# Performance work log

Measured on AMD Instinct MI355X. Metric: run time of the kernel, lower is better.

Reference implementation:

```python
import jax, jax.numpy as jnp
import numpy as np

N, F_IN, H1, H2, HEADS, E = 8192, 512, 128, 64, 3, 262144
NEG_SLOPE = 0.2  # PyG GATConv default negative_slope


def _add_self_loops(src, dst, n):
    loop = jnp.arange(n, dtype=src.dtype)
    return jnp.concatenate([src, loop]), jnp.concatenate([dst, loop])


def _gcn_conv(x, src, dst, W, b, n):
    # PyG GCNConv: h = x @ W, add self-loops, symmetric D^-1/2 A D^-1/2 aggregation, + bias
    h = x @ W
    s, d = _add_self_loops(src, dst, n)
    deg = jax.ops.segment_sum(jnp.ones(s.shape, h.dtype), d, num_segments=n)
    dinv = jnp.where(deg > 0, jax.lax.rsqrt(deg), 0.0)
    norm = dinv[s] * dinv[d]  # [E']
    return jax.ops.segment_sum(h[s] * norm[:, None], d, num_segments=n) + b


def _gat_conv(x, src, dst, W, a_src, a_dst, b, n, heads, concat):
    # PyG GATConv: per-head linear, LeakyReLU attention logits, segment softmax over
    # incoming edges per destination node, weighted scatter-aggregate.
    out_dim = W.shape[1] // heads
    h = (x @ W).reshape(n, heads, out_dim)  # [N, H, D]
    s, d = _add_self_loops(src, dst, n)
    a_s = jnp.einsum('nhd,hd->nh', h, a_src)
    a_d = jnp.einsum('nhd,hd->nh', h, a_dst)
    e = jax.nn.leaky_relu(a_s[s] + a_d[d], NEG_SLOPE)  # [E', H]
    m = jax.ops.segment_max(e, d, num_segments=n)      # stable softmax per dst segment
    ex = jnp.exp(e - m[d])
    den = jax.ops.segment_sum(ex, d, num_segments=n)
    msg = h[s] * (ex / den[d])[..., None]              # [E', H, D]
    out = jax.ops.segment_sum(msg, d, num_segments=n)  # [N, H, D]
    if concat:
        return out.reshape(n, heads * out_dim) + b
    return out.mean(axis=1) + b


def _forward(x, edge_index, gcn_W1, gcn_b1, gcn_Wmu, gcn_bmu, gcn_Wlv, gcn_blv,
             gat_W1, gat_as1, gat_ad1, gat_b1,
             gat_Wmu, gat_asmu, gat_admu, gat_bmu,
             gat_Wlv, gat_aslv, gat_adlv, gat_blv,
             eps_gcn, eps_gat):
    src, dst = edge_index[0], edge_index[1]
    n = x.shape[0]
    mu_g = lv_g = z_g = None
    for i in range(gcn_W1.shape[0]):  # gcn branches
        h = jax.nn.relu(_gcn_conv(x, src, dst, gcn_W1[i], gcn_b1[i], n))
        mu = _gcn_conv(h, src, dst, gcn_Wmu[i], gcn_bmu[i], n)
        lv = _gcn_conv(h, src, dst, gcn_Wlv[i], gcn_blv[i], n)
        z = mu + eps_gcn[i] * jnp.exp(lv)  # faithful: logvar passed as logstd
        mu_g = mu if mu_g is None else jnp.maximum(mu_g, mu)
        lv_g = lv if lv_g is None else jnp.maximum(lv_g, lv)
        z_g = z if z_g is None else jnp.maximum(z_g, z)
    mu_a = lv_a = z_a = None
    for i in range(gat_W1.shape[0]):  # gat branches
        h = jax.nn.relu(_gat_conv(x, src, dst, gat_W1[i], gat_as1[i], gat_ad1[i], gat_b1[i], n, HEADS, True))
        mu = _gat_conv(h, src, dst, gat_Wmu[i], gat_asmu[i], gat_admu[i], gat_bmu[i], n, HEADS, False)
        lv = _gat_conv(h, src, dst, gat_Wlv[i], gat_aslv[i], gat_adlv[i], gat_blv[i], n, HEADS, False)
        z = mu + eps_gat[i] * jnp.exp(lv)
        mu_a = mu if mu_a is None else jnp.maximum(mu_a, mu)
        lv_a = lv if lv_a is None else jnp.maximum(lv_a, lv)
        z_a = z if z_a is None else jnp.maximum(z_a, z)
    mu_max = jnp.maximum(mu_g, mu_a)
    lv_max = jnp.maximum(lv_g, lv_a)
    z_max = jnp.maximum(z_g, z_a)
    adj = jax.nn.sigmoid(z_max @ z_max.T)  # InnerProductDecoder.forward_all(sigmoid=True)
    return adj, mu_max, lv_max


def setup_inputs():
    key = jax.random.key(0)
    ki = iter(jax.random.split(key, 32))
    p = lambda shape: jax.random.normal(next(ki), shape, dtype=jnp.float32) * 0.05
    x = jax.random.normal(next(ki), (N, F_IN), dtype=jnp.float32)
    edge_index = jax.random.randint(next(ki), (2, E), 0, N)
    return dict(
        x=x, edge_index=edge_index,
        gcn_W1=p((2, F_IN, H1)), gcn_b1=p((2, H1)),
        gcn_Wmu=p((2, H1, H2)), gcn_bmu=p((2, H2)),
        gcn_Wlv=p((2, H1, H2)), gcn_blv=p((2, H2)),
        gat_W1=p((2, F_IN, HEADS * H1)), gat_as1=p((2, HEADS, H1)),
        gat_ad1=p((2, HEADS, H1)), gat_b1=p((2, HEADS * H1)),
        gat_Wmu=p((2, HEADS * H1, HEADS * H2)), gat_asmu=p((2, HEADS, H2)),
        gat_admu=p((2, HEADS, H2)), gat_bmu=p((2, H2)),
        gat_Wlv=p((2, HEADS * H1, HEADS * H2)), gat_aslv=p((2, HEADS, H2)),
        gat_adlv=p((2, HEADS, H2)), gat_blv=p((2, H2)),
        eps_gcn=jax.random.normal(next(ki), (2, N, H2), dtype=jnp.float32),
        eps_gat=jax.random.normal(next(ki), (2, N, H2), dtype=jnp.float32),
    )


def reference(x, edge_index, gcn_W1, gcn_b1, gcn_Wmu, gcn_bmu, gcn_Wlv, gcn_blv,
              gat_W1, gat_as1, gat_ad1, gat_b1,
              gat_Wmu, gat_asmu, gat_admu, gat_bmu,
              gat_Wlv, gat_aslv, gat_adlv, gat_blv,
              eps_gcn, eps_gat):
    return _forward(x, edge_index, gcn_W1, gcn_b1, gcn_Wmu, gcn_bmu, gcn_Wlv, gcn_blv,
                    gat_W1, gat_as1, gat_ad1, gat_b1,
                    gat_Wmu, gat_asmu, gat_admu, gat_bmu,
                    gat_Wlv, gat_aslv, gat_adlv, gat_blv,
                    eps_gcn, eps_gat)
```

## Files before the change

kernel.cpp:

```cpp
#include <hip/hip_runtime.h>
#include <hip/hip_bf16.h>
#include <math.h>
#include <stddef.h>

#define NN 8192
#define NEG_SLOPE 0.2f

typedef _Float16 h8 __attribute__((ext_vector_type(8)));
typedef __attribute__((ext_vector_type(4))) float f32x4;

__device__ __forceinline__ float lrelu(float x) { return x > 0.f ? x : NEG_SLOPE * x; }
__device__ __forceinline__ float sigf(float x) { return 1.f / (1.f + __expf(-x)); }

__device__ __forceinline__ unsigned short f16b(float x) {
    _Float16 h = (_Float16)x;
    unsigned short u;
    __builtin_memcpy(&u, &h, 2);
    return u;
}
__device__ __forceinline__ float f16f(unsigned short u) {
    _Float16 h;
    __builtin_memcpy(&h, &u, 2);
    return (float)h;
}
__device__ __forceinline__ void splith(float x, unsigned short& hu, unsigned short& lu) {
    _Float16 h = (_Float16)x;
    float hf = (float)h;
    _Float16 l = (_Float16)(x - hf);
    __builtin_memcpy(&hu, &h, 2);
    __builtin_memcpy(&lu, &l, 2);
}
__device__ __forceinline__ float2 unpkh(unsigned int v) {
    float2 r;
    r.x = f16f((unsigned short)(v & 0xffffu));
    r.y = f16f((unsigned short)(v >> 16));
    return r;
}
__device__ __forceinline__ unsigned int packh(float a, float b) {
    return (unsigned int)f16b(a) | ((unsigned int)f16b(b) << 16);
}

__device__ __forceinline__ void gll16(const unsigned short* g, unsigned short* l) {
    __builtin_amdgcn_global_load_lds(
        (const __attribute__((address_space(1))) unsigned int*)g,
        (__attribute__((address_space(3))) unsigned int*)l, 16, 0, 0);
}

__global__ void k_zero(int* __restrict__ p, int n) {
    int i = blockIdx.x * blockDim.x + threadIdx.x;
    if (i < n) p[i] = 0;
}
__global__ void k_count(const int* __restrict__ dst, int* __restrict__ cnt, int E) {
    int i = blockIdx.x * blockDim.x + threadIdx.x;
    if (i < E) atomicAdd(&cnt[dst[i]], 1);
}
__global__ void k_dinv(const int* __restrict__ cnt, float* __restrict__ dinv) {
    int i = blockIdx.x * blockDim.x + threadIdx.x;
    if (i < NN) dinv[i] = rsqrtf((float)(cnt[i] + 1));
}
__global__ void k_scan(const int* __restrict__ cnt, int* __restrict__ row_ptr) {
    __shared__ int part[1024];
    int t = threadIdx.x;
    int base = t * 8;
    int loc[8];
    int s = 0;
    #pragma unroll
    for (int j = 0; j < 8; ++j) { loc[j] = s; s += cnt[base + j]; }
    part[t] = s;
    __syncthreads();
    for (int off = 1; off < 1024; off <<= 1) {
        int v = (t >= off) ? part[t - off] : 0;
        __syncthreads();
        part[t] += v;
        __syncthreads();
    }
    int pre = (t == 0) ? 0 : part[t - 1];
    #pragma unroll
    for (int j = 0; j < 8; ++j) row_ptr[base + j] = pre + loc[j];
    if (t == 1023) row_ptr[NN] = part[1023];
}
__global__ void k_fill(const int* __restrict__ src, const int* __restrict__ dst,
                       const int* __restrict__ row_ptr, int* __restrict__ cursor,
                       int* __restrict__ csr_src, int E) {
    int i = blockIdx.x * blockDim.x + threadIdx.x;
    if (i < E) {
        int d = dst[i];
        csr_src[row_ptr[d] + atomicAdd(&cursor[d], 1)] = src[i];
    }
}

__global__ void k_cvt_x(const float* __restrict__ x, unsigned short* __restrict__ xh) {
    int i = blockIdx.x * 256 + threadIdx.x;
    int m = i >> 7, k4 = (i & 127) * 4;
    float4 v = *(const float4*)(x + (size_t)m * 512 + k4);
    ushort4 o;
    o.x = f16b(v.x); o.y = f16b(v.y); o.z = f16b(v.z); o.w = f16b(v.w);
    *(ushort4*)&xh[(size_t)m * 512 + k4] = o;
}

__global__ void k_wT(const float* __restrict__ W, unsigned short* __restrict__ Wt,
                     int K, int N, size_t wt_z_stride, int noff, int noff_z) {
    int b = blockIdx.z;
    W += (size_t)b * K * N;
    Wt += (size_t)b * wt_z_stride;
    int rowbase = noff + b * noff_z;
    int k0 = blockIdx.x * 32, n0 = blockIdx.y * 32;
    __shared__ float tl[32][33];
    int tid = threadIdx.x;
    int r = tid >> 5, cc = tid & 31;
    #pragma unroll
    for (int c = 0; c < 4; ++c)
        tl[r + c * 8][cc] = W[(size_t)(k0 + r + c * 8) * N + n0 + cc];
    __syncthreads();
    #pragma unroll
    for (int c = 0; c < 4; ++c) {
        int n = r + c * 8, k = cc;
        Wt[(size_t)(rowbase + n0 + n) * K + k0 + k] = f16b(tl[k][n]);
    }
}

template <int ROWS>
__device__ __forceinline__ void stage(const unsigned short* __restrict__ gbase, int lda,
                                      unsigned short* lds, int wid, int lane) {
    #pragma unroll
    for (int c = 0; c < ROWS / 32; ++c) {
        int chunk = c * 4 + wid;
        int row = chunk * 8 + (lane >> 3);
        int g = (lane & 7) ^ (row & 7);
        gll16(gbase + (size_t)row * lda + g * 8, lds + chunk * 512);
    }
}
__device__ __forceinline__ h8 fragrh(const unsigned short* lds, int row, int kg) {
    return *(const h8*)(lds + row * 64 + ((kg ^ (row & 7)) * 8));
}

template <int TERMS, int EPI>
__global__ __launch_bounds__(256) void k_gemm2(
    const unsigned short* __restrict__ A2, size_t azs, int lda,
    const unsigned short* __restrict__ B2, size_t bzs, int ldb,
    void* __restrict__ Cv, size_t czs, int ldc, int K) {
    __shared__ __align__(16) unsigned short sAh[128 * 64];
    __shared__ __align__(16) unsigned short sBh[64 * 64];
    __shared__ __align__(16) unsigned short sAl[(TERMS == 3) ? 128 * 64 : 8];
    __shared__ __align__(16) unsigned short sBl[(TERMS == 3) ? 64 * 64 : 8];
    const int tid = threadIdx.x;
    const int wid = tid >> 6, lane = tid & 63;
    const int wr = wid >> 1, wc = wid & 1;
    const int lr = lane & 15, lg = lane >> 4;
    const int m0 = blockIdx.x * 128, n0 = blockIdx.y * 64;
    const int z = blockIdx.z;
    A2 += (size_t)z * azs;
    B2 += (size_t)z * bzs;

    const f32x4 zero4 = {0.f, 0.f, 0.f, 0.f};
    f32x4 acc[4][2];
    #pragma unroll
    for (int m = 0; m < 4; ++m)
        #pragma unroll
        for (int n = 0; n < 2; ++n) acc[m][n] = zero4;

    for (int k0 = 0; k0 < K; k0 += 64) {
        stage<128>(A2 + (size_t)m0 * lda + k0, lda, sAh, wid, lane);
        stage<64> (B2 + (size_t)n0 * ldb + k0, ldb, sBh, wid, lane);
        if (TERMS == 3) {
            stage<128>(A2 + (size_t)m0 * lda + K + k0, lda, sAl, wid, lane);
            stage<64> (B2 + (size_t)n0 * ldb + K + k0, ldb, sBl, wid, lane);
        }
        __syncthreads();
        #pragma unroll
        for (int ks = 0; ks < 2; ++ks) {
            const int kg = ks * 4 + lg;
            h8 ah[4], al[4], bh[2], bl[2];
            #pragma unroll
            for (int m = 0; m < 4; ++m) {
                int row = wr * 64 + m * 16 + lr;
                ah[m] = fragrh(sAh, row, kg);
                if (TERMS == 3) al[m] = fragrh(sAl, row, kg);
            }
            #pragma unroll
            for (int n = 0; n < 2; ++n) {
                int row = wc * 32 + n * 16 + lr;
                bh[n] = fragrh(sBh, row, kg);
                if (TERMS == 3) bl[n] = fragrh(sBl, row, kg);
            }
            #pragma unroll
            for (int m = 0; m < 4; ++m)
                #pragma unroll
                for (int n = 0; n < 2; ++n) {
                    acc[m][n] = __builtin_amdgcn_mfma_f32_16x16x32_f16(ah[m], bh[n], acc[m][n], 0, 0, 0);
                    if (TERMS == 3) {
                        acc[m][n] = __builtin_amdgcn_mfma_f32_16x16x32_f16(al[m], bh[n], acc[m][n], 0, 0, 0);
                        acc[m][n] = __builtin_amdgcn_mfma_f32_16x16x32_f16(ah[m], bl[n], acc[m][n], 0, 0, 0);
                    }
                }
        }
        __syncthreads();
    }
    #pragma unroll
    for (int m = 0; m < 4; ++m)
        #pragma unroll
        for (int n = 0; n < 2; ++n)
            #pragma unroll
            for (int j = 0; j < 4; ++j) {
                int row = m0 + wr * 64 + m * 16 + lg * 4 + j;
                int col = n0 + wc * 32 + n * 16 + lr;
                float o = acc[m][n][j];
                if (EPI == 1) {
                    ((float*)Cv + (size_t)z * czs)[(size_t)row * ldc + col] = sigf(o);
                } else if (EPI == 2) {
                    ((unsigned short*)Cv + (size_t)z * czs)[(size_t)row * ldc + col] = f16b(o);
                } else {
                    ((float*)Cv + (size_t)z * czs)[(size_t)row * ldc + col] = o;
                }
            }
}

__global__ void k_gcn_a1(const uint2* __restrict__ xw2, const float* __restrict__ dinv,
                         const int* __restrict__ rp, const int* __restrict__ cs,
                         const float* __restrict__ b1, uint2* __restrict__ hb2) {
    int d = blockIdx.x;
    int t = threadIdx.x;
    float dd = dinv[d];
    uint2 sv = xw2[(size_t)d * 64 + t];
    float2 s0 = unpkh(sv.x), s1 = unpkh(sv.y);
    float a0 = dd * s0.x, a1 = dd * s0.y, a2 = dd * s1.x, a3 = dd * s1.y;
    int e0 = rp[d], e1 = rp[d + 1];
    int j = e0;
    for (; j + 4 <= e1; j += 4) {
        int i0 = cs[j], i1 = cs[j + 1], i2 = cs[j + 2], i3 = cs[j + 3];
        float w0 = dinv[i0], w1 = dinv[i1], w2 = dinv[i2], w3 = dinv[i3];
        uint2 v0 = xw2[(size_t)i0 * 64 + t];
        uint2 v1 = xw2[(size_t)i1 * 64 + t];
        uint2 v2 = xw2[(size_t)i2 * 64 + t];
        uint2 v3 = xw2[(size_t)i3 * 64 + t];
        float2 p;
        p = unpkh(v0.x); a0 += w0 * p.x; a1 += w0 * p.y;
        p = unpkh(v0.y); a2 += w0 * p.x; a3 += w0 * p.y;
        p = unpkh(v1.x); a0 += w1 * p.x; a1 += w1 * p.y;
        p = unpkh(v1.y); a2 += w1 * p.x; a3 += w1 * p.y;
        p = unpkh(v2.x); a0 += w2 * p.x; a1 += w2 * p.y;
        p = unpkh(v2.y); a2 += w2 * p.x; a3 += w2 * p.y;
        p = unpkh(v3.x); a0 += w3 * p.x; a1 += w3 * p.y;
        p = unpkh(v3.y); a2 += w3 * p.x; a3 += w3 * p.y;
    }
    for (; j < e1; ++j) {
        int s = cs[j];
        float w = dinv[s];
        uint2 v = xw2[(size_t)s * 64 + t];
        float2 p;
        p = unpkh(v.x); a0 += w * p.x; a1 += w * p.y;
        p = unpkh(v.y); a2 += w * p.x; a3 += w * p.y;
    }
    int c = 4 * t;
    float o0 = fmaxf(dd * a0 + b1[c], 0.f);
    float o1 = fmaxf(dd * a1 + b1[c + 1], 0.f);
    float o2 = fmaxf(dd * a2 + b1[c + 2], 0.f);
    float o3 = fmaxf(dd * a3 + b1[c + 3], 0.f);
    uint2 o;
    o.x = packh(o0, o1);
    o.y = packh(o2, o3);
    hb2[(size_t)d * 64 + t] = o;
}

__global__ void k_gcn_a2(const uint2* __restrict__ hb2, const float* __restrict__ dinv,
                         const int* __restrict__ rp, const int* __restrict__ cs,
                         uint2* __restrict__ hA2) {
    int d = blockIdx.x;
    int t = threadIdx.x;
    float dd = dinv[d];
    uint2 sv = hb2[(size_t)d * 64 + t];
    float2 s0 = unpkh(sv.x), s1 = unpkh(sv.y);
    float a0 = dd * s0.x, a1 = dd * s0.y, a2 = dd * s1.x, a3 = dd * s1.y;
    int e0 = rp[d], e1 = rp[d + 1];
    int j = e0;
    for (; j + 4 <= e1; j += 4) {
        int i0 = cs[j], i1 = cs[j + 1], i2 = cs[j + 2], i3 = cs[j + 3];
        float w0 = dinv[i0], w1 = dinv[i1], w2 = dinv[i2], w3 = dinv[i3];
        uint2 v0 = hb2[(size_t)i0 * 64 + t];
        uint2 v1 = hb2[(size_t)i1 * 64 + t];
        uint2 v2 = hb2[(size_t)i2 * 64 + t];
        uint2 v3 = hb2[(size_t)i3 * 64 + t];
        float2 p;
        p = unpkh(v0.x); a0 += w0 * p.x; a1 += w0 * p.y;
        p = unpkh(v0.y); a2 += w0 * p.x; a3 += w0 * p.y;
        p = unpkh(v1.x); a0 += w1 * p.x; a1 += w1 * p.y;
        p = unpkh(v1.y); a2 += w1 * p.x; a3 += w1 * p.y;
        p = unpkh(v2.x); a0 += w2 * p.x; a1 += w2 * p.y;
        p = unpkh(v2.y); a2 += w2 * p.x; a3 += w2 * p.y;
        p = unpkh(v3.x); a0 += w3 * p.x; a1 += w3 * p.y;
        p = unpkh(v3.y); a2 += w3 * p.x; a3 += w3 * p.y;
    }
    for (; j < e1; ++j) {
        int s = cs[j];
        float w = dinv[s];
        uint2 v = hb2[(size_t)s * 64 + t];
        float2 p;
        p = unpkh(v.x); a0 += w * p.x; a1 += w * p.y;
        p = unpkh(v.y); a2 += w * p.x; a3 += w * p.y;
    }
    uint2 o;
    o.x = packh(dd * a0, dd * a1);
    o.y = packh(dd * a2, dd * a3);
    hA2[(size_t)d * 64 + t] = o;
}

__global__ void k_gat_log1(const unsigned int* __restrict__ xwu, const float* __restrict__ a_s,
                           const float* __restrict__ a_d, float* __restrict__ as_n,
                           float* __restrict__ ad_n) {
    int br = blockIdx.z;
    int n = blockIdx.x;
    int hd = threadIdx.x >> 6, lane = threadIdx.x & 63;
    const unsigned int* hp = xwu + (size_t)n * 384 + br * 192 + hd * 64;
    const float* av = a_s + br * 384 + hd * 128;
    const float* dv = a_d + br * 384 + hd * 128;
    float2 f = unpkh(hp[lane]);
    float ss = f.x * av[2 * lane] + f.y * av[2 * lane + 1];
    float sd = f.x * dv[2 * lane] + f.y * dv[2 * lane + 1];
    #pragma unroll
    for (int off = 32; off; off >>= 1) {
        ss += __shfl_down(ss, off);
        sd += __shfl_down(sd, off);
    }
    if (lane == 0) {
        as_n[(size_t)br * NN * 3 + n * 3 + hd] = ss;
        ad_n[(size_t)br * NN * 3 + n * 3 + hd] = sd;
    }
}

__global__ void k_gat_log2(const unsigned short* __restrict__ h2gb, const float* __restrict__ asmu,
                           const float* __restrict__ aslv, const float* __restrict__ admu,
                           const float* __restrict__ adlv, float* __restrict__ as_n,
                           float* __restrict__ ad_n) {
    int zz = blockIdx.z;
    int br = zz >> 1, mt = zz & 1;
    int n = blockIdx.x;
    int hd = threadIdx.x >> 6, lane = threadIdx.x & 63;
    const unsigned short* hp = h2gb + (size_t)br * NN * 384 + (size_t)n * 384 + mt * 192 + hd * 64;
    const float* av = (mt ? aslv : asmu) + br * 192 + hd * 64;
    const float* dv = (mt ? adlv : admu) + br * 192 + hd * 64;
    float hv = f16f(hp[lane]);
    float ss = hv * av[lane];
    float sd = hv * dv[lane];
    #pragma unroll
    for (int off = 32; off; off >>= 1) {
        ss += __shfl_down(ss, off);
        sd += __shfl_down(sd, off);
    }
    if (lane == 0) {
        as_n[(size_t)zz * NN * 3 + n * 3 + hd] = ss;
        ad_n[(size_t)zz * NN * 3 + n * 3 + hd] = sd;
    }
}

__global__ void k_gat_attn(const float* __restrict__ as_n, const float* __restrict__ ad_n,
                           const int* __restrict__ rp, const int* __restrict__ cs,
                           float* __restrict__ w_csr, float* __restrict__ w_self, int E3) {
    int zz = blockIdx.z;
    as_n += (size_t)zz * NN * 3;
    ad_n += (size_t)zz * NN * 3;
    w_csr += (size_t)zz * E3;
    w_self += (size_t)zz * NN * 3;
    int d = blockIdx.x;
    int hd = threadIdx.x >> 6, lane = threadIdx.x & 63;
    int e0 = rp[d], e1 = rp[d + 1];
    float add = ad_n[d * 3 + hd];
    float eself = lrelu(as_n[d * 3 + hd] + add);
    float mx = eself;
    for (int j = e0 + lane; j < e1; j += 64) {
        float e = lrelu(as_n[cs[j] * 3 + hd] + add);
        w_csr[(size_t)j * 3 + hd] = e;
        mx = fmaxf(mx, e);
    }
    #pragma unroll
    for (int off = 32; off; off >>= 1) mx = fmaxf(mx, __shfl_xor(mx, off));
    float sm = (lane == 0) ? __expf(eself - mx) : 0.f;
    for (int j = e0 + lane; j < e1; j += 64)
        sm += __expf(w_csr[(size_t)j * 3 + hd] - mx);
    #pragma unroll
    for (int off = 32; off; off >>= 1) sm += __shfl_xor(sm, off);
    float inv = 1.f / sm;
    if (lane == 0) w_self[d * 3 + hd] = __expf(eself - mx) * inv;
    for (int j = e0 + lane; j < e1; j += 64)
        w_csr[(size_t)j * 3 + hd] = __expf(w_csr[(size_t)j * 3 + hd] - mx) * inv;
}

__global__ void k_gat_agg1(const uint2* __restrict__ xw2, const float* __restrict__ w_csr,
                           const float* __restrict__ w_self, const int* __restrict__ rp,
                           const int* __restrict__ cs, const float* __restrict__ b1,
                           uint2* __restrict__ h1s2, int E3) {
    int d = blockIdx.x;
    int t = threadIdx.x;
    int br = t >= 96 ? 1 : 0;
    int c = 4 * t - br * 384;
    int hd = c >> 7;
    const float* wc = w_csr + (size_t)br * E3;
    float ws = w_self[(size_t)br * NN * 3 + d * 3 + hd];
    uint2 sv = xw2[(size_t)d * 192 + t];
    float2 s0 = unpkh(sv.x), s1 = unpkh(sv.y);
    float a0 = ws * s0.x, a1 = ws * s0.y, a2 = ws * s1.x, a3 = ws * s1.y;
    int e0 = rp[d], e1 = rp[d + 1];
    int j = e0;
    for (; j + 4 <= e1; j += 4) {
        int i0 = cs[j], i1 = cs[j + 1], i2 = cs[j + 2], i3 = cs[j + 3];
        float w0 = wc[(size_t)(j + 0) * 3 + hd];
        float w1 = wc[(size_t)(j + 1) * 3 + hd];
        float w2 = wc[(size_t)(j + 2) * 3 + hd];
        float w3 = wc[(size_t)(j + 3) * 3 + hd];
        uint2 v0 = xw2[(size_t)i0 * 192 + t];
        uint2 v1 = xw2[(size_t)i1 * 192 + t];
        uint2 v2 = xw2[(size_t)i2 * 192 + t];
        uint2 v3 = xw2[(size_t)i3 * 192 + t];
        float2 p;
        p = unpkh(v0.x); a0 += w0 * p.x; a1 += w0 * p.y;
        p = unpkh(v0.y); a2 += w0 * p.x; a3 += w0 * p.y;
        p = unpkh(v1.x); a0 += w1 * p.x; a1 += w1 * p.y;
        p = unpkh(v1.y); a2 += w1 * p.x; a3 += w1 * p.y;
        p = unpkh(v2.x); a0 += w2 * p.x; a1 += w2 * p.y;
        p = unpkh(v2.y); a2 += w2 * p.x; a3 += w2 * p.y;
        p = unpkh(v3.x); a0 += w3 * p.x; a1 += w3 * p.y;
        p = unpkh(v3.y); a2 += w3 * p.x; a3 += w3 * p.y;
    }
    for (; j < e1; ++j) {
        int s = cs[j];
        float w = wc[(size_t)j * 3 + hd];
        uint2 v = xw2[(size_t)s * 192 + t];
        float2 p;
        p = unpkh(v.x); a0 += w * p.x; a1 += w * p.y;
        p = unpkh(v.y); a2 += w * p.x; a3 += w * p.y;
    }
    int cg = 4 * t;
    float o0 = fmaxf(a0 + b1[cg], 0.f);
    float o1 = fmaxf(a1 + b1[cg + 1], 0.f);
    float o2 = fmaxf(a2 + b1[cg + 2], 0.f);
    float o3 = fmaxf(a3 + b1[cg + 3], 0.f);
    uint2 o;
    o.x = packh(o0, o1);
    o.y = packh(o2, o3);
    h1s2[(size_t)d * 192 + t] = o;
}

__global__ void k_gat_agg2(const uint2* __restrict__ h2g2, const float* __restrict__ w_csr,
                           const float* __restrict__ w_self, const int* __restrict__ rp,
                           const int* __restrict__ cs, const float* __restrict__ bmu,
                           const float* __restrict__ blv, float* __restrict__ mt_gat, int E3) {
    int d = blockIdx.x;
    int t = threadIdx.x;
    int br = t >= 96 ? 1 : 0;
    int tb = t - br * 96;
    int mt = tb >= 48 ? 1 : 0;
    int c = 4 * tb - mt * 192;
    int hd = c >> 6;
    const float* wc = w_csr + (size_t)(br * 2 + mt) * E3;
    float ws = w_self[(size_t)(br * 2 + mt) * NN * 3 + d * 3 + hd];
    const uint2* hp = h2g2 + (size_t)br * NN * 96;
    uint2 sv = hp[(size_t)d * 96 + tb];
    float2 s0 = unpkh(sv.x), s1 = unpkh(sv.y);
    float a0 = ws * s0.x, a1 = ws * s0.y, a2 = ws * s1.x, a3 = ws * s1.y;
    int e0 = rp[d], e1 = rp[d + 1];
    int j = e0;
    for (; j + 4 <= e1; j += 4) {
        int i0 = cs[j], i1 = cs[j + 1], i2 = cs[j + 2], i3 = cs[j + 3];
        float w0 = wc[(size_t)(j + 0) * 3 + hd];
        float w1 = wc[(size_t)(j + 1) * 3 + hd];
        float w2 = wc[(size_t)(j + 2) * 3 + hd];
        float w3 = wc[(size_t)(j + 3) * 3 + hd];
        uint2 v0 = hp[(size_t)i0 * 96 + tb];
        uint2 v1 = hp[(size_t)i1 * 96 + tb];
        uint2 v2 = hp[(size_t)i2 * 96 + tb];
        uint2 v3 = hp[(size_t)i3 * 96 + tb];
        float2 p;
        p = unpkh(v0.x); a0 += w0 * p.x; a1 += w0 * p.y;
        p = unpkh(v0.y); a2 += w0 * p.x; a3 += w0 * p.y;
        p = unpkh(v1.x); a0 += w1 * p.x; a1 += w1 * p.y;
        p = unpkh(v1.y); a2 += w1 * p.x; a3 += w1 * p.y;
        p = unpkh(v2.x); a0 += w2 * p.x; a1 += w2 * p.y;
        p = unpkh(v2.y); a2 += w2 * p.x; a3 += w2 * p.y;
        p = unpkh(v3.x); a0 += w3 * p.x; a1 += w3 * p.y;
        p = unpkh(v3.y); a2 += w3 * p.x; a3 += w3 * p.y;
    }
    for (; j < e1; ++j) {
        int s = cs[j];
        float w = wc[(size_t)j * 3 + hd];
        uint2 v = hp[(size_t)s * 96 + tb];
        float2 p;
        p = unpkh(v.x); a0 += w * p.x; a1 += w * p.y;
        p = unpkh(v.y); a2 += w * p.x; a3 += w * p.y;
    }
    __shared__ float red[768];
    int rb = br * 384 + mt * 192 + c;
    red[rb] = a0; red[rb + 1] = a1; red[rb + 2] = a2; red[rb + 3] = a3;
    __syncthreads();
    if (t < 128) {
        #pragma unroll
        for (int q = 0; q < 2; ++q) {
            int o = t + q * 128;
            int obr = o >> 7, omt = (o >> 6) & 1, dd = o & 63;
            int base = obr * 384 + omt * 192;
            float tot = red[base + dd] + red[base + 64 + dd] + red[base + 128 + dd];
            const float* bias = omt ? blv : bmu;
            float v = tot * (1.f / 3.f) + bias[obr * 64 + dd];
            mt_gat[((size_t)(obr * 2 + omt) * NN + d) * 64 + dd] = v;
        }
    }
}

__global__ void k_finalize(const float* __restrict__ muv_gcn, const float* __restrict__ gcn_bmu,
                           const float* __restrict__ gcn_blv, const float* __restrict__ mt_gat,
                           const float* __restrict__ eps_gcn, const float* __restrict__ eps_gat,
                           float* __restrict__ mu_o, float* __restrict__ lv_o,
                           unsigned short* __restrict__ z2) {
    int i = blockIdx.x * 256 + threadIdx.x;
    int d = i >> 6, c = i & 63;
    const size_t NN64 = (size_t)NN * 64;
    float mu, lv, zm;
    {
        float m = muv_gcn[(size_t)d * 128 + c] + gcn_bmu[c];
        float l = muv_gcn[(size_t)d * 128 + 64 + c] + gcn_blv[c];
        float z = m + eps_gcn[i] * __expf(l);
        mu = m; lv = l; zm = z;
    }
    {
        float m = muv_gcn[NN64 * 2 + (size_t)d * 128 + c] + gcn_bmu[64 + c];
        float l = muv_gcn[NN64 * 2 + (size_t)d * 128 + 64 + c] + gcn_blv[64 + c];
        float z = m + eps_gcn[NN64 + i] * __expf(l);
        mu = fmaxf(mu, m); lv = fmaxf(lv, l); zm = fmaxf(zm, z);
    }
    #pragma unroll
    for (int br = 0; br < 2; ++br) {
        float m = mt_gat[(size_t)(br * 2 + 0) * NN64 + i];
        float l = mt_gat[(size_t)(br * 2 + 1) * NN64 + i];
        float z = m + eps_gat[(size_t)br * NN64 + i] * __expf(l);
        mu = fmaxf(mu, m); lv = fmaxf(lv, l); zm = fmaxf(zm, z);
    }
    mu_o[i] = mu;
    lv_o[i] = lv;
    unsigned short hh, ll;
    splith(zm, hh, ll);
    z2[(size_t)d * 128 + c] = hh;
    z2[(size_t)d * 128 + 64 + c] = ll;
}

extern "C" void kernel_launch(void* const* d_in, const int* in_sizes, int n_in,
                              void* d_out, int out_size, void* d_ws, size_t ws_size,
                              hipStream_t stream) {
    const float* x  = (const float*)d_in[0];
    const int*   ei = (const int*)d_in[1];
    const int E = in_sizes[1] / 2;
    const int E3 = E * 3;
    const int* src = ei;
    const int* dst = ei + E;

    const float* gcn_W1  = (const float*)d_in[2];
    const float* gcn_b1  = (const float*)d_in[3];
    const float* gcn_Wmu = (const float*)d_in[4];
    const float* gcn_bmu = (const float*)d_in[5];
    const float* gcn_Wlv = (const float*)d_in[6];
    const float* gcn_blv = (const float*)d_in[7];
    const float* gat_W1  = (const float*)d_in[8];
    const float* gat_as1 = (const float*)d_in[9];
    const float* gat_ad1 = (const float*)d_in[10];
    const float* gat_b1  = (const float*)d_in[11];
    const float* gat_Wmu = (const float*)d_in[12];
    const float* gat_asmu= (const float*)d_in[13];
    const float* gat_admu= (const float*)d_in[14];
    const float* gat_bmu = (const float*)d_in[15];
    const float* gat_Wlv = (const float*)d_in[16];
    const float* gat_aslv= (const float*)d_in[17];
    const float* gat_adlv= (const float*)d_in[18];
    const float* gat_blv = (const float*)d_in[19];
    const float* eps_gcn = (const float*)d_in[20];
    const float* eps_gat = (const float*)d_in[21];

    char* p = (char*)d_ws;
    auto alloc = [&](size_t bytes) {
        void* r = (void*)p;
        p += (bytes + 255) & ~(size_t)255;
        return r;
    };
    int*   cnt     = (int*)alloc((size_t)NN * 4);
    int*   cursor  = (int*)alloc((size_t)NN * 4);
    int*   row_ptr = (int*)alloc((size_t)(NN + 1) * 4);
    int*   csr_src = (int*)alloc((size_t)E * 4);
    float* dinv    = (float*)alloc((size_t)NN * 4);
    float* as_n1   = (float*)alloc((size_t)2 * NN * 3 * 4);
    float* ad_n1   = (float*)alloc((size_t)2 * NN * 3 * 4);
    float* wself1  = (float*)alloc((size_t)2 * NN * 3 * 4);
    float* wcsr1   = (float*)alloc((size_t)2 * E3 * 4);
    float* as_n2   = (float*)alloc((size_t)4 * NN * 3 * 4);
    float* ad_n2   = (float*)alloc((size_t)4 * NN * 3 * 4);
    float* wself2  = (float*)alloc((size_t)4 * NN * 3 * 4);
    float* wcsr2   = (float*)alloc((size_t)4 * E3 * 4);
    unsigned short* x2h      = (unsigned short*)alloc((size_t)NN * 512 * 2);
    unsigned short* wt_gcn1  = (unsigned short*)alloc((size_t)256 * 512 * 2);
    unsigned short* wt_gcnmuv= (unsigned short*)alloc((size_t)2 * 128 * 128 * 2);
    unsigned short* wt_gat1  = (unsigned short*)alloc((size_t)768 * 512 * 2);
    unsigned short* wt_gatmuv= (unsigned short*)alloc((size_t)2 * 384 * 384 * 2);
    unsigned short* xwb  = (unsigned short*)alloc((size_t)NN * 768 * 2);
    unsigned short* hb   = (unsigned short*)alloc((size_t)NN * 256 * 2);
    unsigned short* hA   = (unsigned short*)alloc((size_t)NN * 256 * 2);
    float* muv_gcn = (float*)alloc((size_t)2 * NN * 128 * 4);
    unsigned short* h1s  = (unsigned short*)alloc((size_t)NN * 768 * 2);
    unsigned short* h2gb = (unsigned short*)alloc((size_t)2 * NN * 384 * 2);
    float* mt_gat  = (float*)alloc((size_t)4 * NN * 64 * 4);
    unsigned short* z2 = (unsigned short*)alloc((size_t)NN * 128 * 2);

    float* adj  = (float*)d_out;
    float* mu_o = adj + (size_t)NN * NN;
    float* lv_o = mu_o + (size_t)NN * 64;

    k_zero<<<(2 * NN + 255) / 256, 256, 0, stream>>>(cnt, 2 * NN);
    k_count<<<(E + 255) / 256, 256, 0, stream>>>(dst, cnt, E);
    k_dinv<<<(NN + 255) / 256, 256, 0, stream>>>(cnt, dinv);
    k_scan<<<1, 1024, 0, stream>>>(cnt, row_ptr);
    k_fill<<<(E + 255) / 256, 256, 0, stream>>>(src, dst, row_ptr, cursor, csr_src, E);

    k_cvt_x<<<NN * 512 / 4 / 256, 256, 0, stream>>>(x, x2h);
    k_wT<<<dim3(16, 4, 2), 256, 0, stream>>>(gcn_W1, wt_gcn1, 512, 128, 0, 0, 128);
    k_wT<<<dim3(4, 2, 2), 256, 0, stream>>>(gcn_Wmu, wt_gcnmuv, 128, 64, (size_t)128 * 128, 0, 0);
    k_wT<<<dim3(4, 2, 2), 256, 0, stream>>>(gcn_Wlv, wt_gcnmuv, 128, 64, (size_t)128 * 128, 64, 0);
    k_wT<<<dim3(16, 12, 2), 256, 0, stream>>>(gat_W1, wt_gat1, 512, 384, 0, 0, 384);
    k_wT<<<dim3(12, 6, 2), 256, 0, stream>>>(gat_Wmu, wt_gatmuv, 384, 192, (size_t)384 * 384, 0, 0);
    k_wT<<<dim3(12, 6, 2), 256, 0, stream>>>(gat_Wlv, wt_gatmuv, 384, 192, (size_t)384 * 384, 192, 0);

    k_gemm2<1, 2><<<dim3(64, 4, 1), 256, 0, stream>>>(x2h, 0, 512, wt_gcn1, 0, 512,
                                                      xwb, 0, 256, 512);
    k_gcn_a1<<<NN, 64, 0, stream>>>((const uint2*)xwb, dinv, row_ptr, csr_src, gcn_b1,
                                    (uint2*)hb);
    k_gcn_a2<<<NN, 64, 0, stream>>>((const uint2*)hb, dinv, row_ptr, csr_src, (uint2*)hA);
    k_gemm2<1, 0><<<dim3(64, 2, 2), 256, 0, stream>>>(hA, 128, 256, wt_gcnmuv,
                                                      (size_t)128 * 128, 128,
                                                      muv_gcn, (size_t)NN * 128, 128, 128);

    k_gemm2<1, 2><<<dim3(64, 12, 1), 256, 0, stream>>>(x2h, 0, 512, wt_gat1, 0, 512,
                                                       xwb, 0, 768, 512);
    k_gat_log1<<<dim3(NN, 1, 2), 192, 0, stream>>>((const unsigned int*)xwb, gat_as1,
                                                   gat_ad1, as_n1, ad_n1);
    k_gat_attn<<<dim3(NN, 1, 2), 192, 0, stream>>>(as_n1, ad_n1, row_ptr, csr_src,
                                                   wcsr1, wself1, E3);
    k_gat_agg1<<<NN, 192, 0, stream>>>((const uint2*)xwb, wcsr1, wself1, row_ptr, csr_src,
                                       gat_b1, (uint2*)h1s, E3);
    k_gemm2<1, 2><<<dim3(64, 6, 2), 256, 0, stream>>>(h1s, 384, 768, wt_gatmuv,
                                                      (size_t)384 * 384, 384,
                                                      h2gb, (size_t)NN * 384, 384, 384);
    k_gat_log2<<<dim3(NN, 1, 4), 192, 0, stream>>>(h2gb, gat_asmu, gat_aslv, gat_admu,
                                                   gat_adlv, as_n2, ad_n2);
    k_gat_attn<<<dim3(NN, 1, 4), 192, 0, stream>>>(as_n2, ad_n2, row_ptr, csr_src,
                                                   wcsr2, wself2, E3);
    k_gat_agg2<<<NN, 192, 0, stream>>>((const uint2*)h2gb, wcsr2, wself2, row_ptr, csr_src,
                                       gat_bmu, gat_blv, mt_gat, E3);

    k_finalize<<<NN * 64 / 256, 256, 0, stream>>>(muv_gcn, gcn_bmu, gcn_blv, mt_gat,
                                                  eps_gcn, eps_gat, mu_o, lv_o, z2);
    k_gemm2<3, 1><<<dim3(64, 128, 1), 256, 0, stream>>>(z2, 0, 128, z2, 0, 128,
                                                        adj, 0, NN, 64);
}
```

Before: 364.8 us.

## Split neighbor gathers across thread groups with 16-byte loads and LDS reduction

Result: slower. 376.1 us (+3.1%).

```diff
diff --git a/kernel.cpp b/kernel.cpp
--- a/kernel.cpp
+++ b/kernel.cpp
@@ -38,6 +38,13 @@
 }
 __device__ __forceinline__ unsigned int packh(float a, float b) {
     return (unsigned int)f16b(a) | ((unsigned int)f16b(b) << 16);
+}
+__device__ __forceinline__ void acc8(float* a, uint4 v, float w) {
+    float2 p;
+    p = unpkh(v.x); a[0] += w * p.x; a[1] += w * p.y;
+    p = unpkh(v.y); a[2] += w * p.x; a[3] += w * p.y;
+    p = unpkh(v.z); a[4] += w * p.x; a[5] += w * p.y;
+    p = unpkh(v.w); a[6] += w * p.x; a[7] += w * p.y;
 }
 
 __device__ __forceinline__ void gll16(const unsigned short* g, unsigned short* l) {
@@ -215,93 +222,53 @@
             }
 }
 
-__global__ void k_gcn_a1(const uint2* __restrict__ xw2, const float* __restrict__ dinv,
-                         const int* __restrict__ rp, const int* __restrict__ cs,
-                         const float* __restrict__ b1, uint2* __restrict__ hb2) {
+template <int RELU_BIAS>
+__global__ void k_gcn_agg(const uint4* __restrict__ v4, const float* __restrict__ dinv,
+                          const int* __restrict__ rp, const int* __restrict__ cs,
+                          const float* __restrict__ b1, unsigned int* __restrict__ outu) {
     int d = blockIdx.x;
     int t = threadIdx.x;
+    int g = t >> 5, lr = t & 31;
     float dd = dinv[d];
-    uint2 sv = xw2[(size_t)d * 64 + t];
-    float2 s0 = unpkh(sv.x), s1 = unpkh(sv.y);
-    float a0 = dd * s0.x, a1 = dd * s0.y, a2 = dd * s1.x, a3 = dd * s1.y;
+    float a[8] = {0.f, 0.f, 0.f, 0.f, 0.f, 0.f, 0.f, 0.f};
+    if (g == 0) {
+        uint4 sv = v4[(size_t)d * 32 + lr];
+        acc8(a, sv, dd);
+    }
     int e0 = rp[d], e1 = rp[d + 1];
-    int j = e0;
-    for (; j + 4 <= e1; j += 4) {
-        int i0 = cs[j], i1 = cs[j + 1], i2 = cs[j + 2], i3 = cs[j + 3];
-        float w0 = dinv[i0], w1 = dinv[i1], w2 = dinv[i2], w3 = dinv[i3];
-        uint2 v0 = xw2[(size_t)i0 * 64 + t];
-        uint2 v1 = xw2[(size_t)i1 * 64 + t];
-        uint2 v2 = xw2[(size_t)i2 * 64 + t];
-        uint2 v3 = xw2[(size_t)i3 * 64 + t];
-        float2 p;
-        p = unpkh(v0.x); a0 += w0 * p.x; a1 += w0 * p.y;
-        p = unpkh(v0.y); a2 += w0 * p.x; a3 += w0 * p.y;
-        p = unpkh(v1.x); a0 += w1 * p.x; a1 += w1 * p.y;
-        p = unpkh(v1.y); a2 += w1 * p.x; a3 += w1 * p.y;
-        p = unpkh(v2.x); a0 += w2 * p.x; a1 += w2 * p.y;
-        p = unpkh(v2.y); a2 += w2 * p.x; a3 += w2 * p.y;
-        p = unpkh(v3.x); a0 += w3 * p.x; a1 += w3 * p.y;
-        p = unpkh(v3.y); a2 += w3 * p.x; a3 += w3 * p.y;
-    }
-    for (; j < e1; ++j) {
+    int j = e0 + g;
+    for (; j + 8 < e1; j += 16) {
+        int s0 = cs[j], s1 = cs[j + 8];
+        float w0 = dinv[s0], w1 = dinv[s1];
+        uint4 v0 = v4[(size_t)s0 * 32 + lr];
+        uint4 v1 = v4[(size_t)s1 * 32 + lr];
+        acc8(a, v0, w0);
+        acc8(a, v1, w1);
+    }
+    if (j < e1) {
         int s = cs[j];
-        float w = dinv[s];
-        uint2 v = xw2[(size_t)s * 64 + t];
-        float2 p;
-        p = unpkh(v.x); a0 += w * p.x; a1 += w * p.y;
-        p = unpkh(v.y); a2 += w * p.x; a3 += w * p.y;
-    }
-    int c = 4 * t;
-    float o0 = fmaxf(dd * a0 + b1[c], 0.f);
-    float o1 = fmaxf(dd * a1 + b1[c + 1], 0.f);
-    float o2 = fmaxf(dd * a2 + b1[c + 2], 0.f);
-    float o3 = fmaxf(dd * a3 + b1[c + 3], 0.f);
-    uint2 o;
-    o.x = packh(o0, o1);
-    o.y = packh(o2, o3);
-    hb2[(size_t)d * 64 + t] = o;
-}
-
-__global__ void k_gcn_a2(const uint2* __restrict__ hb2, const float* __restrict__ dinv,
-                         const int* __restrict__ rp, const int* __restrict__ cs,
-                         uint2* __restrict__ hA2) {
-    int d = blockIdx.x;
-    int t = threadIdx.x;
-    float dd = dinv[d];
-    uint2 sv = hb2[(size_t)d * 64 + t];
-    float2 s0 = unpkh(sv.x), s1 = unpkh(sv.y);
-    float a0 = dd * s0.x, a1 = dd * s0.y, a2 = dd * s1.x, a3 = dd * s1.y;
-    int e0 = rp[d], e1 = rp[d + 1];
-    int j = e0;
-    for (; j + 4 <= e1; j += 4) {
-        int i0 = cs[j], i1 = cs[j + 1], i2 = cs[j + 2], i3 = cs[j + 3];
-        float w0 = dinv[i0], w1 = dinv[i1], w2 = dinv[i2], w3 = dinv[i3];
-        uint2 v0 = hb2[(size_t)i0 * 64 + t];
-        uint2 v1 = hb2[(size_t)i1 * 64 + t];
-        uint2 v2 = hb2[(size_t)i2 * 64 + t];
-        uint2 v3 = hb2[(size_t)i3 * 64 + t];
-        float2 p;
-        p = unpkh(v0.x); a0 += w0 * p.x; a1 += w0 * p.y;
-        p = unpkh(v0.y); a2 += w0 * p.x; a3 += w0 * p.y;
-        p = unpkh(v1.x); a0 += w1 * p.x; a1 += w1 * p.y;
-        p = unpkh(v1.y); a2 += w1 * p.x; a3 += w1 * p.y;
-        p = unpkh(v2.x); a0 += w2 * p.x; a1 += w2 * p.y;
-        p = unpkh(v2.y); a2 += w2 * p.x; a3 += w2 * p.y;
-        p = unpkh(v3.x); a0 += w3 * p.x; a1 += w3 * p.y;
-        p = unpkh(v3.y); a2 += w3 * p.x; a3 += w3 * p.y;
-    }
-    for (; j < e1; ++j) {
-        int s = cs[j];
-        float w = dinv[s];
-        uint2 v = hb2[(size_t)s * 64 + t];
-        float2 p;
-        p = unpkh(v.x); a0 += w * p.x; a1 += w * p.y;
-        p = unpkh(v.y); a2 += w * p.x; a3 += w * p.y;
-    }
-    uint2 o;
-    o.x = packh(dd * a0, dd * a1);
-    o.y = packh(dd * a2, dd * a3);
-    hA2[(size_t)d * 64 + t] = o;
+        uint4 v = v4[(size_t)s * 32 + lr];
+        acc8(a, v, dinv[s]);
+    }
+    __shared__ float red[8][256];
+    #pragma unroll
+    for (int i = 0; i < 8; ++i) red[g][lr * 8 + i] = a[i];
+    __syncthreads();
+    if (t < 128) {
+        int c0 = 2 * t, c1 = 2 * t + 1;
+        float s0 = 0.f, s1 = 0.f;
+        #pragma unroll
+        for (int gg = 0; gg < 8; ++gg) { s0 += red[gg][c0]; s1 += red[gg][c1]; }
+        float o0, o1;
+        if (RELU_BIAS) {
+            o0 = fmaxf(dd * s0 + b1[c0], 0.f);
+            o1 = fmaxf(dd * s1 + b1[c1], 0.f);
+        } else {
+            o0 = dd * s0;
+            o1 = dd * s1;
+        }
+        outu[(size_t)d * 128 + t] = packh(o0, o1);
+    }
 }
 
 __global__ void k_gat_log1(const unsigned int* __restrict__ xwu, const float* __restrict__ a_s,
@@ -384,123 +351,107 @@
         w_csr[(size_t)j * 3 + hd] = __expf(w_csr[(size_t)j * 3 + hd] - mx) * inv;
 }
 
-__global__ void k_gat_agg1(const uint2* __restrict__ xw2, const float* __restrict__ w_csr,
+__global__ void k_gat_agg1(const uint4* __restrict__ xw4, const float* __restrict__ w_csr,
                            const float* __restrict__ w_self, const int* __restrict__ rp,
                            const int* __restrict__ cs, const float* __restrict__ b1,
-                           uint2* __restrict__ h1s2, int E3) {
+                           unsigned int* __restrict__ h1su, int E3) {
     int d = blockIdx.x;
     int t = threadIdx.x;
-    int br = t >= 96 ? 1 : 0;
-    int c = 4 * t - br * 384;
-    int hd = c >> 7;
+    int g = t / 96, lr = t - g * 96;
+    int c = lr * 8;
+    int br = c >= 384 ? 1 : 0;
+    int cb = c - br * 384;
+    int hd = cb >> 7;
     const float* wc = w_csr + (size_t)br * E3;
-    float ws = w_self[(size_t)br * NN * 3 + d * 3 + hd];
-    uint2 sv = xw2[(size_t)d * 192 + t];
-    float2 s0 = unpkh(sv.x), s1 = unpkh(sv.y);
-    float a0 = ws * s0.x, a1 = ws * s0.y, a2 = ws * s1.x, a3 = ws * s1.y;
+    float a[8] = {0.f, 0.f, 0.f, 0.f, 0.f, 0.f, 0.f, 0.f};
+    if (g == 0) {
+        float ws = w_self[(size_t)br * NN * 3 + d * 3 + hd];
+        uint4 sv = xw4[(size_t)d * 96 + lr];
+        acc8(a, sv, ws);
+    }
     int e0 = rp[d], e1 = rp[d + 1];
-    int j = e0;
-    for (; j + 4 <= e1; j += 4) {
-        int i0 = cs[j], i1 = cs[j + 1], i2 = cs[j + 2], i3 = cs[j + 3];
-        float w0 = wc[(size_t)(j + 0) * 3 + hd];
-        float w1 = wc[(size_t)(j + 1) * 3 + hd];
-        float w2 = wc[(size_t)(j + 2) * 3 + hd];
-        float w3 = wc[(size_t)(j + 3) * 3 + hd];
-        uint2 v0 = xw2[(size_t)i0 * 192 + t];
-        uint2 v1 = xw2[(size_t)i1 * 192 + t];
-        uint2 v2 = xw2[(size_t)i2 * 192 + t];
-        uint2 v3 = xw2[(size_t)i3 * 192 + t];
-        float2 p;
-        p = unpkh(v0.x); a0 += w0 * p.x; a1 += w0 * p.y;
-        p = unpkh(v0.y); a2 += w0 * p.x; a3 += w0 * p.y;
-        p = unpkh(v1.x); a0 += w1 * p.x; a1 += w1 * p.y;
-        p = unpkh(v1.y); a2 += w1 * p.x; a3 += w1 * p.y;
-        p = unpkh(v2.x); a0 += w2 * p.x; a1 += w2 * p.y;
-        p = unpkh(v2.y); a2 += w2 * p.x; a3 += w2 * p.y;
-        p = unpkh(v3.x); a0 += w3 * p.x; a1 += w3 * p.y;
-        p = unpkh(v3.y); a2 += w3 * p.x; a3 += w3 * p.y;
-    }
-    for (; j < e1; ++j) {
+    int j = e0 + g;
+    for (; j + 4 < e1; j += 8) {
+        int s0 = cs[j], s1 = cs[j + 4];
+        float w0 = wc[(size_t)j * 3 + hd];
+        float w1 = wc[(size_t)(j + 4) * 3 + hd];
+        uint4 v0 = xw4[(size_t)s0 * 96 + lr];
+        uint4 v1 = xw4[(size_t)s1 * 96 + lr];
+        acc8(a, v0, w0);
+        acc8(a, v1, w1);
+    }
+    if (j < e1) {
         int s = cs[j];
         float w = wc[(size_t)j * 3 + hd];
-        uint2 v = xw2[(size_t)s * 192 + t];
-        float2 p;
-        p = unpkh(v.x); a0 += w * p.x; a1 += w * p.y;
-        p = unpkh(v.y); a2 += w * p.x; a3 += w * p.y;
-    }
-    int cg = 4 * t;
-    float o0 = fmaxf(a0 + b1[cg], 0.f);
-    float o1 = fmaxf(a1 + b1[cg + 1], 0.f);
-    float o2 = fmaxf(a2 + b1[cg + 2], 0.f);
-    float o3 = fmaxf(a3 + b1[cg + 3], 0.f);
-    uint2 o;
-    o.x = packh(o0, o1);
-    o.y = packh(o2, o3);
-    h1s2[(size_t)d * 192 + t] = o;
-}
-
-__global__ void k_gat_agg2(const uint2* __restrict__ h2g2, const float* __restrict__ w_csr,
+        uint4 v = xw4[(size_t)s * 96 + lr];
+        acc8(a, v, w);
+    }
+    __shared__ float red[4][768];
+    #pragma unroll
+    for (int i = 0; i < 8; ++i) red[g][c + i] = a[i];
+    __syncthreads();
+    {
+        int c0 = 2 * t, c1 = 2 * t + 1;
+        float s0 = 0.f, s1 = 0.f;
+        #pragma unroll
+        for (int gg = 0; gg < 4; ++gg) { s0 += red[gg][c0]; s1 += red[gg][c1]; }
+        float o0 = fmaxf(s0 + b1[c0], 0.f);
+        float o1 = fmaxf(s1 + b1[c1], 0.f);
+        h1su[(size_t)d * 384 + t] = packh(o0, o1);
+    }
+}
+
+__global__ void k_gat_agg2(const uint4* __restrict__ h2g4, const float* __restrict__ w_csr,
                            const float* __restrict__ w_self, const int* __restrict__ rp,
                            const int* __restrict__ cs, const float* __restrict__ bmu,
                            const float* __restrict__ blv, float* __restrict__ mt_gat, int E3) {
     int d = blockIdx.x;
     int t = threadIdx.x;
-    int br = t >= 96 ? 1 : 0;
-    int tb = t - br * 96;
-    int mt = tb >= 48 ? 1 : 0;
-    int c = 4 * tb - mt * 192;
-    int hd = c >> 6;
+    int g = t / 96, lr = t - g * 96;
+    int br = lr / 48, li = lr - br * 48;
+    int c = li * 8;
+    int mt = c >= 192 ? 1 : 0;
+    int cm = c - mt * 192;
+    int hd = cm >> 6;
     const float* wc = w_csr + (size_t)(br * 2 + mt) * E3;
-    float ws = w_self[(size_t)(br * 2 + mt) * NN * 3 + d * 3 + hd];
-    const uint2* hp = h2g2 + (size_t)br * NN * 96;
-    uint2 sv = hp[(size_t)d * 96 + tb];
-    float2 s0 = unpkh(sv.x), s1 = unpkh(sv.y);
-    float a0 = ws * s0.x, a1 = ws * s0.y, a2 = ws * s1.x, a3 = ws * s1.y;
+    const uint4* hp = h2g4 + (size_t)br * NN * 48;
+    float a[8] = {0.f, 0.f, 0.f, 0.f, 0.f, 0.f, 0.f, 0.f};
+    if (g == 0) {
+        float ws = w_self[(size_t)(br * 2 + mt) * NN * 3 + d * 3 + hd];
+        uint4 sv = hp[(size_t)d * 48 + li];
+        acc8(a, sv, ws);
+    }
     int e0 = rp[d], e1 = rp[d + 1];
-    int j = e0;
-    for (; j + 4 <= e1; j += 4) {
-        int i0 = cs[j], i1 = cs[j + 1], i2 = cs[j + 2], i3 = cs[j + 3];
-        float w0 = wc[(size_t)(j + 0) * 3 + hd];
-        float w1 = wc[(size_t)(j + 1) * 3 + hd];
-        float w2 = wc[(size_t)(j + 2) * 3 + hd];
-        float w3 = wc[(size_t)(j + 3) * 3 + hd];
-        uint2 v0 = hp[(size_t)i0 * 96 + tb];
-        uint2 v1 = hp[(size_t)i1 * 96 + tb];
-        uint2 v2 = hp[(size_t)i2 * 96 + tb];
-        uint2 v3 = hp[(size_t)i3 * 96 + tb];
-        float2 p;
-        p = unpkh(v0.x); a0 += w0 * p.x; a1 += w0 * p.y;
-        p = unpkh(v0.y); a2 += w0 * p.x; a3 += w0 * p.y;
-        p = unpkh(v1.x); a0 += w1 * p.x; a1 += w1 * p.y;
-        p = unpkh(v1.y); a2 += w1 * p.x; a3 += w1 * p.y;
-        p = unpkh(v2.x); a0 += w2 * p.x; a1 += w2 * p.y;
-        p = unpkh(v2.y); a2 += w2 * p.x; a3 += w2 * p.y;
-        p = unpkh(v3.x); a0 += w3 * p.x; a1 += w3 * p.y;
-        p = unpkh(v3.y); a2 += w3 * p.x; a3 += w3 * p.y;
-    }
-    for (; j < e1; ++j) {
+    int j = e0 + g;
+    for (; j + 4 < e1; j += 8) {
+        int s0 = cs[j], s1 = cs[j + 4];
+        float w0 = wc[(size_t)j * 3 + hd];
+        float w1 = wc[(size_t)(j + 4) * 3 + hd];
+        uint4 v0 = hp[(size_t)s0 * 48 + li];
+        uint4 v1 = hp[(size_t)s1 * 48 + li];
+        acc8(a, v0, w0);
+        acc8(a, v1, w1);
+    }
+    if (j < e1) {
         int s = cs[j];
         float w = wc[(size_t)j * 3 + hd];
-        uint2 v = hp[(size_t)s * 96 + tb];
-        float2 p;
-        p = unpkh(v.x); a0 += w * p.x; a1 += w * p.y;
-        p = unpkh(v.y); a2 += w * p.x; a3 += w * p.y;
-    }
-    __shared__ float red[768];
-    int rb = br * 384 + mt * 192 + c;
-    red[rb] = a0; red[rb + 1] = a1; red[rb + 2] = a2; red[rb + 3] = a3;
+        uint4 v = hp[(size_t)s * 48 + li];
+        acc8(a, v, w);
+    }
+    __shared__ float red[4][768];
+    #pragma unroll
+    for (int i = 0; i < 8; ++i) red[g][br * 384 + c + i] = a[i];
     __syncthreads();
-    if (t < 128) {
+    if (t < 256) {
+        int obr = t >> 7, omt = (t >> 6) & 1, dd2 = t & 63;
+        int base = obr * 384 + omt * 192;
+        float tot = 0.f;
         #pragma unroll
-        for (int q = 0; q < 2; ++q) {
-            int o = t + q * 128;
-            int obr = o >> 7, omt = (o >> 6) & 1, dd = o & 63;
-            int base = obr * 384 + omt * 192;
-            float tot = red[base + dd] + red[base + 64 + dd] + red[base + 128 + dd];
-            const float* bias = omt ? blv : bmu;
-            float v = tot * (1.f / 3.f) + bias[obr * 64 + dd];
-            mt_gat[((size_t)(obr * 2 + omt) * NN + d) * 64 + dd] = v;
-        }
+        for (int gg = 0; gg < 4; ++gg)
+            tot += red[gg][base + dd2] + red[gg][base + 64 + dd2] + red[gg][base + 128 + dd2];
+        const float* bias = omt ? blv : bmu;
+        float v = tot * (1.f / 3.f) + bias[obr * 64 + dd2];
+        mt_gat[((size_t)(obr * 2 + omt) * NN + d) * 64 + dd2] = v;
     }
 }
 
@@ -624,9 +575,10 @@
 
     k_gemm2<1, 2><<<dim3(64, 4, 1), 256, 0, stream>>>(x2h, 0, 512, wt_gcn1, 0, 512,
                                                       xwb, 0, 256, 512);
-    k_gcn_a1<<<NN, 64, 0, stream>>>((const uint2*)xwb, dinv, row_ptr, csr_src, gcn_b1,
-                                    (uint2*)hb);
-    k_gcn_a2<<<NN, 64, 0, stream>>>((const uint2*)hb, dinv, row_ptr, csr_src, (uint2*)hA);
+    k_gcn_agg<1><<<NN, 256, 0, stream>>>((const uint4*)xwb, dinv, row_ptr, csr_src,
+                                         gcn_b1, (unsigned int*)hb);
+    k_gcn_agg<0><<<NN, 256, 0, stream>>>((const uint4*)hb, dinv, row_ptr, csr_src,
+                                         nullptr, (unsigned int*)hA);
     k_gemm2<1, 0><<<dim3(64, 2, 2), 256, 0, stream>>>(hA, 128, 256, wt_gcnmuv,
                                                       (size_t)128 * 128, 128,
                                                       muv_gcn, (size_t)NN * 128, 128, 128);
@@ -637,8 +589,8 @@
                                                    gat_ad1, as_n1, ad_n1);
     k_gat_attn<<<dim3(NN, 1, 2), 192, 0, stream>>>(as_n1, ad_n1, row_ptr, csr_src,
                                                    wcsr1, wself1, E3);
-    k_gat_agg1<<<NN, 192, 0, stream>>>((const uint2*)xwb, wcsr1, wself1, row_ptr, csr_src,
-                                       gat_b1, (uint2*)h1s, E3);
+    k_gat_agg1<<<NN, 384, 0, stream>>>((const uint4*)xwb, wcsr1, wself1, row_ptr, csr_src,
+                                       gat_b1, (unsigned int*)h1s, E3);
     k_gemm2<1, 2><<<dim3(64, 6, 2), 256, 0, stream>>>(h1s, 384, 768, wt_gatmuv,
                                                       (size_t)384 * 384, 384,
                                                       h2gb, (size_t)NN * 384, 384, 384);
@@ -646,7 +598,7 @@
                                                    gat_adlv, as_n2, ad_n2);
     k_gat_attn<<<dim3(NN, 1, 4), 192, 0, stream>>>(as_n2, ad_n2, row_ptr, csr_src,
                                                    wcsr2, wself2, E3);
-    k_gat_agg2<<<NN, 192, 0, stream>>>((const uint2*)h2gb, wcsr2, wself2, row_ptr, csr_src,
+    k_gat_agg2<<<NN, 384, 0, stream>>>((const uint4*)h2gb, wcsr2, wself2, row_ptr, csr_src,
                                        gat_bmu, gat_blv, mt_gat, E3);
 
     k_finalize<<<NN * 64 / 256, 256, 0, stream>>>(muv_gcn, gcn_bmu, gcn_blv, mt_gat,
```
